# Optimization experiments

Hardware: AMD Instinct MI355X
Metric: run time of the kernel (lower is better)

Reference implementation:

```python
import jax, jax.numpy as jnp
import numpy as np
import math

INPUT_DIM = 256
HIDDEN_DIM = 128  # per-head dim
NUM_HEAD = 8
N = 1024          # seq len == variables
BATCH = 8
C = HIDDEN_DIM * NUM_HEAD  # 1024


def setup_inputs() -> dict:
    key = jax.random.key(0)
    ks = jax.random.split(key, 11)
    s = 0.02
    return {
        "x": jax.random.normal(ks[0], (BATCH, N, INPUT_DIM), dtype=jnp.float32),
        "B_bias": jax.random.normal(ks[1], (N, N), dtype=jnp.float32),
        "wq_w": jax.random.normal(ks[2], (INPUT_DIM, C), dtype=jnp.float32) * s,
        "wq_b": jax.random.normal(ks[3], (C,), dtype=jnp.float32) * s,
        "wk_w": jax.random.normal(ks[4], (INPUT_DIM, C), dtype=jnp.float32) * s,
        "wk_b": jax.random.normal(ks[5], (C,), dtype=jnp.float32) * s,
        "wv_w": jax.random.normal(ks[6], (INPUT_DIM, C), dtype=jnp.float32) * s,
        "wv_b": jax.random.normal(ks[7], (C,), dtype=jnp.float32) * s,
        "proj_w": jax.random.normal(ks[8], (C, HIDDEN_DIM), dtype=jnp.float32) * s,
        "proj_b": jax.random.normal(ks[9], (HIDDEN_DIM,), dtype=jnp.float32) * s,
    }


def reference(x, B_bias, wq_w, wq_b, wk_w, wk_b, wv_w, wv_b, proj_w, proj_b):
    B, n, _ = x.shape
    sdk = jnp.float32(math.sqrt(HIDDEN_DIM))
    # projections -> [B, N, C], split heads -> [B, H, N, h]
    def heads(y):
        return y.reshape(B, n, NUM_HEAD, HIDDEN_DIM).transpose(0, 2, 1, 3)
    q = heads(x @ wq_w + wq_b)
    k = heads(x @ wk_w + wk_b)
    v = heads(x @ wv_w + wv_b)
    # scores [B, H, N, N] with learned additive bias (broadcast over B, H)
    scores = jnp.einsum("bhnd,bhmd->bhnm", q, k) / sdk + B_bias
    attn = jax.nn.softmax(scores, axis=-1)
    out = jnp.einsum("bhnm,bhmd->bhnd", attn, v)  # [B, H, N, h]
    out = out.transpose(0, 2, 1, 3).reshape(B, n, C)
    return out @ proj_w + proj_b
```

## Files before the change

kernel.cpp:

```cpp
#include <hip/hip_runtime.h>
#include <math.h>

#define SEQ  1024
#define IND  256
#define CC   1024
#define NH   8
#define HD   128
#define BH   64

typedef __bf16 bf16x8 __attribute__((ext_vector_type(8)));
typedef __bf16 bf16x4 __attribute__((ext_vector_type(4)));
typedef float  f32x4  __attribute__((ext_vector_type(4)));
typedef unsigned short u16;

static constexpr float RSDK = 0.08838834764831845f;

__device__ __forceinline__ u16 f2bf(float f) {
    unsigned int u = __float_as_uint(f);
    u += 0x7fffu + ((u >> 16) & 1u);
    return (u16)(u >> 16);
}

__global__ __launch_bounds__(256) void prep_kernel(
    const float* __restrict__ x, u16* __restrict__ xb,
    const float* __restrict__ w0, const float* __restrict__ w1, const float* __restrict__ w2,
    u16* __restrict__ o0, u16* __restrict__ o1, u16* __restrict__ o2,
    const float* __restrict__ pw, u16* __restrict__ pT)
{
    __shared__ float tile[32][33];
    const int id = blockIdx.x;

    if (id < 2048) {
        const int i = id * 256 + threadIdx.x;
        float4 v = ((const float4*)x)[i];
        ushort4 o;
        o.x = f2bf(v.x); o.y = f2bf(v.y); o.z = f2bf(v.z); o.w = f2bf(v.w);
        ((ushort4*)xb)[i] = o;
        return;
    }

    const float* in; u16* out; int R, C, c0, r0;
    if (id < 2816) {
        const int rem = id - 2048;
        const int z = rem >> 8;
        const int rem2 = rem & 255;
        in  = (z == 0) ? w0 : (z == 1) ? w1 : w2;
        out = (z == 0) ? o0 : (z == 1) ? o1 : o2;
        R = IND; C = CC;
        c0 = (rem2 & 31) * 32;
        r0 = (rem2 >> 5) * 32;
    } else {
        const int rem = id - 2816;
        in = pw; out = pT;
        R = CC; C = HD;
        c0 = (rem & 3) * 32;
        r0 = (rem >> 2) * 32;
    }

    const int row = threadIdx.x >> 3, col4 = (threadIdx.x & 7) * 4;
    float4 v = *(const float4*)&in[(size_t)(r0 + row) * C + c0 + col4];
    tile[row][col4 + 0] = v.x; tile[row][col4 + 1] = v.y;
    tile[row][col4 + 2] = v.z; tile[row][col4 + 3] = v.w;
    __syncthreads();
    ushort4 o;
    o.x = f2bf(tile[col4 + 0][row]);
    o.y = f2bf(tile[col4 + 1][row]);
    o.z = f2bf(tile[col4 + 2][row]);
    o.w = f2bf(tile[col4 + 3][row]);
    *(ushort4*)&out[(size_t)(c0 + row) * R + r0 + col4] = o;
}

#define QKV_LDW 72
__global__ __launch_bounds__(256) void qkv_kernel(
    const u16* __restrict__ xb,
    const u16* __restrict__ wT0, const u16* __restrict__ wT1, const u16* __restrict__ wT2,
    const float* __restrict__ b0, const float* __restrict__ b1, const float* __restrict__ b2,
    u16* __restrict__ q_out, u16* __restrict__ k_out, u16* __restrict__ vt_out)
{
    const int mat = blockIdx.z;
    const u16* wT  = (mat == 0) ? wT0 : (mat == 1) ? wT1 : wT2;
    const float* wb = (mat == 0) ? b0 : (mat == 1) ? b1 : b2;
    const float scale = (mat == 0) ? RSDK : 1.0f;

    __shared__ __align__(16) u16 As[128 * QKV_LDW];
    __shared__ __align__(16) u16 Bs[128 * QKV_LDW];

    const int tid = threadIdx.x;
    const int lane = tid & 63, wave = tid >> 6;
    const int ln = lane & 15, quad = lane >> 4;
    const int m0 = blockIdx.x * 128;
    const int n0 = blockIdx.y * 128;
    const int wm = (wave & 1) * 64;
    const int wn = (wave >> 1) * 64;

    f32x4 acc[4][4];
    #pragma unroll
    for (int mb = 0; mb < 4; ++mb)
        #pragma unroll
        for (int nb = 0; nb < 4; ++nb)
            #pragma unroll
            for (int r = 0; r < 4; ++r) acc[mb][nb][r] = 0.0f;

    const int r8 = tid >> 3, pb8 = tid & 7;

    const u16* ag = xb + (size_t)(m0 + r8) * IND + pb8 * 8;
    const u16* bg = wT + (size_t)(n0 + r8) * IND + pb8 * 8;

    bf16x8 pa[4], pbv[4];
    #pragma unroll
    for (int c = 0; c < 4; ++c) {
        pa[c]  = *(const bf16x8*)(ag + (size_t)c * 32 * IND);
        pbv[c] = *(const bf16x8*)(bg + (size_t)c * 32 * IND);
    }

    for (int kt = 0; kt < 4; ++kt) {
        __syncthreads();
        #pragma unroll
        for (int c = 0; c < 4; ++c) {
            *(bf16x8*)(As + (size_t)(c * 32 + r8) * QKV_LDW + pb8 * 8) = pa[c];
            *(bf16x8*)(Bs + (size_t)(c * 32 + r8) * QKV_LDW + pb8 * 8) = pbv[c];
        }
        __syncthreads();
        if (kt < 3) {
            #pragma unroll
            for (int c = 0; c < 4; ++c) {
                pa[c]  = *(const bf16x8*)(ag + (size_t)c * 32 * IND + (kt + 1) * 64);
                pbv[c] = *(const bf16x8*)(bg + (size_t)c * 32 * IND + (kt + 1) * 64);
            }
        }
        #pragma unroll
        for (int ks = 0; ks < 2; ++ks) {
            bf16x8 af[4], bf[4];
            #pragma unroll
            for (int mb = 0; mb < 4; ++mb)
                af[mb] = *(const bf16x8*)(As + (size_t)(wm + mb * 16 + ln) * QKV_LDW
                                             + (ks * 4 + quad) * 8);
            #pragma unroll
            for (int nb = 0; nb < 4; ++nb)
                bf[nb] = *(const bf16x8*)(Bs + (size_t)(wn + nb * 16 + ln) * QKV_LDW
                                             + (ks * 4 + quad) * 8);
            #pragma unroll
            for (int mb = 0; mb < 4; ++mb)
                #pragma unroll
                for (int nb = 0; nb < 4; ++nb)
                    acc[mb][nb] = __builtin_amdgcn_mfma_f32_16x16x32_bf16(
                        af[mb], bf[nb], acc[mb][nb], 0, 0, 0);
        }
    }

    if (mat != 2) {
        u16* outp = (mat == 0) ? q_out : k_out;
        #pragma unroll
        for (int nb = 0; nb < 4; ++nb) {
            const int c = n0 + wn + nb * 16 + ln;
            const float bv = wb[c];
            const int h = c >> 7, d = c & 127;
            #pragma unroll
            for (int mb = 0; mb < 4; ++mb) {
                #pragma unroll
                for (int r = 0; r < 4; ++r) {
                    const int m = m0 + wm + mb * 16 + quad * 4 + r;
                    const int b = m >> 10, tok = m & 1023;
                    outp[((size_t)(b * NH + h) * SEQ + tok) * HD + d] =
                        f2bf((acc[mb][nb][r] + bv) * scale);
                }
            }
        }
    } else {
        #pragma unroll
        for (int nb = 0; nb < 4; ++nb) {
            const int c = n0 + wn + nb * 16 + ln;
            const float bv = wb[c];
            const int h = c >> 7, d = c & 127;
            #pragma unroll
            for (int mb = 0; mb < 4; ++mb) {
                const int m = m0 + wm + mb * 16 + quad * 4;
                const int b = m >> 10, tok0 = m & 1023;
                ushort4 o;
                o.x = f2bf(acc[mb][nb][0] + bv);
                o.y = f2bf(acc[mb][nb][1] + bv);
                o.z = f2bf(acc[mb][nb][2] + bv);
                o.w = f2bf(acc[mb][nb][3] + bv);
                *(ushort4*)&vt_out[((size_t)(b * NH + h) * HD + d) * SEQ + tok0] = o;
            }
        }
    }
}

#define KVB    32
#define KS_LDW 136
#define VS_LDW 40
#define PL_LDW 36
__global__ __launch_bounds__(256) void attn_kernel(
    const u16* __restrict__ Q, const u16* __restrict__ K,
    const u16* __restrict__ Vt, const float* __restrict__ bias,
    u16* __restrict__ aout)
{
    __shared__ __align__(16) u16 Ks[KVB * KS_LDW];
    __shared__ __align__(16) u16 Vs[128 * VS_LDW];
    __shared__ __align__(16) u16 Pl[4][16 * PL_LDW];

    const int tid = threadIdx.x;
    const int lane = tid & 63, wave = tid >> 6;
    const int ln = lane & 15, quad = lane >> 4;
    const int bh = blockIdx.x;
    const int q0 = blockIdx.y * 64 + wave * 16;

    bf16x8 qf[4];
    {
        const u16* qp = Q + ((size_t)bh * SEQ + q0 + ln) * HD + quad * 8;
        #pragma unroll
        for (int ks = 0; ks < 4; ++ks) qf[ks] = *(const bf16x8*)(qp + ks * 32);
    }

    f32x4 Oa[8];
    #pragma unroll
    for (int db = 0; db < 8; ++db)
        #pragma unroll
        for (int r = 0; r < 4; ++r) Oa[db][r] = 0.0f;
    float l_i[4] = {0.0f, 0.0f, 0.0f, 0.0f};

    u16* ppw = &Pl[wave][0];
    const u16* Kg0 = K  + (size_t)bh * SEQ * HD;
    const u16* Vg0 = Vt + (size_t)bh * HD * SEQ;
    const float* brow0 = bias + (size_t)(q0 + quad * 4) * SEQ + ln;

    const int r16 = tid >> 4, pb16 = tid & 15;
    const int r4  = tid >> 2, pb4  = tid & 3;

    const u16* kg = Kg0 + (size_t)r16 * HD + pb16 * 8;
    const u16* vg = Vg0 + (size_t)r4 * SEQ + pb4 * 8;

    bf16x8 kp[2], vp[2];
    #pragma unroll
    for (int c = 0; c < 2; ++c) {
        kp[c] = *(const bf16x8*)(kg + (size_t)c * 16 * HD);
        vp[c] = *(const bf16x8*)(vg + (size_t)c * 64 * SEQ);
    }

    float bpre[2][4];
    #pragma unroll
    for (int nb = 0; nb < 2; ++nb)
        #pragma unroll
        for (int r = 0; r < 4; ++r)
            bpre[nb][r] = brow0[(size_t)r * SEQ + nb * 16];

    for (int kt = 0; kt < 32; ++kt) {
        __syncthreads();
        #pragma unroll
        for (int c = 0; c < 2; ++c) {
            *(bf16x8*)(Ks + (size_t)(c * 16 + r16) * KS_LDW + pb16 * 8) = kp[c];
            *(bf16x8*)(Vs + (size_t)(c * 64 + r4) * VS_LDW + pb4 * 8)   = vp[c];
        }
        __syncthreads();

        if (kt < 31) {
            #pragma unroll
            for (int c = 0; c < 2; ++c) {
                kp[c] = *(const bf16x8*)(kg + (size_t)(kt + 1) * KVB * HD + (size_t)c * 16 * HD);
                vp[c] = *(const bf16x8*)(vg + (size_t)c * 64 * SEQ + (kt + 1) * KVB);
            }
        }

        #pragma unroll
        for (int nb = 0; nb < 2; ++nb) {
            const u16* kr = Ks + (size_t)(nb * 16 + ln) * KS_LDW;
            bf16x8 kf[4];
            #pragma unroll
            for (int ks = 0; ks < 4; ++ks)
                kf[ks] = *(const bf16x8*)(kr + (ks * 4 + quad) * 8);
            f32x4 s;
            #pragma unroll
            for (int r = 0; r < 4; ++r) s[r] = 0.0f;
            #pragma unroll
            for (int ks = 0; ks < 4; ++ks)
                s = __builtin_amdgcn_mfma_f32_16x16x32_bf16(qf[ks], kf[ks], s, 0, 0, 0);
            #pragma unroll
            for (int r = 0; r < 4; ++r) {
                const float p = __expf(s[r] + bpre[nb][r]);
                l_i[r] += p;
                ppw[(quad * 4 + r) * PL_LDW + nb * 16 + ln] = f2bf(p);
            }
        }

        if (kt < 31) {
            #pragma unroll
            for (int nb = 0; nb < 2; ++nb)
                #pragma unroll
                for (int r = 0; r < 4; ++r)
                    bpre[nb][r] = brow0[(size_t)r * SEQ + (kt + 1) * KVB + nb * 16];
        }

        bf16x8 af;
        {
            const u16* pr = ppw + ln * PL_LDW + quad * 8;
            bf16x4 lo = *(const bf16x4*)(pr);
            bf16x4 hi = *(const bf16x4*)(pr + 4);
            #pragma unroll
            for (int j = 0; j < 4; ++j) { af[j] = lo[j]; af[4 + j] = hi[j]; }
        }

        #pragma unroll
        for (int db = 0; db < 8; ++db) {
            bf16x8 vf = *(const bf16x8*)(Vs + (size_t)(db * 16 + ln) * VS_LDW + quad * 8);
            Oa[db] = __builtin_amdgcn_mfma_f32_16x16x32_bf16(af, vf, Oa[db], 0, 0, 0);
        }
    }

    const int b = bh >> 3, h = bh & 7;
    #pragma unroll
    for (int r = 0; r < 4; ++r) {
        float v = l_i[r];
        #pragma unroll
        for (int off = 1; off < 16; off <<= 1) v += __shfl_xor(v, off);
        const float inv = 1.0f / v;
        const int tok = q0 + quad * 4 + r;
        u16* op = aout + ((size_t)(b * SEQ + tok)) * CC + h * HD + ln;
        #pragma unroll
        for (int db = 0; db < 8; ++db) op[db * 16] = f2bf(Oa[db][r] * inv);
    }
}

__global__ __launch_bounds__(256) void proj_kernel(
    const u16* __restrict__ A, const u16* __restrict__ pT,
    const float* __restrict__ pb, float* __restrict__ out)
{
    __shared__ float Rs[3][16 * 132];
    const int tid = threadIdx.x;
    const int lane = tid & 63, kh = tid >> 6;
    const int ln = lane & 15, quad = lane >> 4;
    const int m0 = blockIdx.x * 16;

    f32x4 acc[8];
    #pragma unroll
    for (int nb = 0; nb < 8; ++nb)
        #pragma unroll
        for (int r = 0; r < 4; ++r) acc[nb][r] = 0.0f;

    const u16* ap = A  + (size_t)(m0 + ln) * CC + kh * 256 + quad * 8;
    const u16* bp = pT + (size_t)ln * CC + kh * 256 + quad * 8;

    #pragma unroll
    for (int kt = 0; kt < 8; ++kt) {
        bf16x8 af = *(const bf16x8*)(ap + kt * 32);
        #pragma unroll
        for (int nb = 0; nb < 8; ++nb) {
            bf16x8 bf = *(const bf16x8*)(bp + (size_t)nb * 16 * CC + kt * 32);
            acc[nb] = __builtin_amdgcn_mfma_f32_16x16x32_bf16(af, bf, acc[nb], 0, 0, 0);
        }
    }

    if (kh > 0) {
        #pragma unroll
        for (int nb = 0; nb < 8; ++nb)
            #pragma unroll
            for (int r = 0; r < 4; ++r)
                Rs[kh - 1][(quad * 4 + r) * 132 + nb * 16 + ln] = acc[nb][r];
    }
    __syncthreads();
    if (kh == 0) {
        #pragma unroll
        for (int nb = 0; nb < 8; ++nb) {
            const int c = nb * 16 + ln;
            const float bv = pb[c];
            #pragma unroll
            for (int r = 0; r < 4; ++r) {
                const int ri = (quad * 4 + r) * 132 + c;
                out[(size_t)(m0 + quad * 4 + r) * HD + c] =
                    acc[nb][r] + Rs[0][ri] + Rs[1][ri] + Rs[2][ri] + bv;
            }
        }
    }
}

extern "C" void kernel_launch(void* const* d_in, const int* in_sizes, int n_in,
                              void* d_out, int out_size, void* d_ws, size_t ws_size,
                              hipStream_t stream)
{
    const float* x    = (const float*)d_in[0];
    const float* bias = (const float*)d_in[1];
    const float* wq   = (const float*)d_in[2];
    const float* wqb  = (const float*)d_in[3];
    const float* wk   = (const float*)d_in[4];
    const float* wkb  = (const float*)d_in[5];
    const float* wv   = (const float*)d_in[6];
    const float* wvb  = (const float*)d_in[7];
    const float* pw   = (const float*)d_in[8];
    const float* pb   = (const float*)d_in[9];
    float* out = (float*)d_out;

    u16* ws = (u16*)d_ws;
    size_t off = 0;
    u16* xb  = ws + off; off += (size_t)8192 * IND;
    u16* wqT = ws + off; off += (size_t)CC * IND;
    u16* wkT = ws + off; off += (size_t)CC * IND;
    u16* wvT = ws + off; off += (size_t)CC * IND;
    u16* pT  = ws + off; off += (size_t)HD * CC;
    u16* Qw  = ws + off; off += (size_t)BH * SEQ * HD;
    u16* Kw  = ws + off; off += (size_t)BH * SEQ * HD;
    u16* Vtw = ws + off; off += (size_t)BH * HD * SEQ;
    u16* Aw  = ws + off; off += (size_t)8192 * CC;

    prep_kernel<<<2944, 256, 0, stream>>>(x, xb, wq, wk, wv, wqT, wkT, wvT, pw, pT);
    qkv_kernel<<<dim3(64, 8, 3), 256, 0, stream>>>(
        xb, wqT, wkT, wvT, wqb, wkb, wvb, Qw, Kw, Vtw);
    attn_kernel<<<dim3(64, 16), 256, 0, stream>>>(Qw, Kw, Vtw, bias, Aw);
    proj_kernel<<<512, 256, 0, stream>>>(Aw, pT, pb, out);
}
```

Baseline: 190.3 us.

## Transpose QK^T MFMA and build P operand in registers via permlane swaps

```diff
diff --git a/kernel.cpp b/kernel.cpp
--- a/kernel.cpp
+++ b/kernel.cpp
@@ -19,6 +19,12 @@
     unsigned int u = __float_as_uint(f);
     u += 0x7fffu + ((u >> 16) & 1u);
     return (u16)(u >> 16);
+}
+
+__device__ __forceinline__ unsigned cvt_pk_bf16(float lo, float hi) {
+    unsigned r;
+    asm("v_cvt_pk_bf16_f32 %0, %1, %2" : "=v"(r) : "v"(lo), "v"(hi));
+    return r;
 }
 
 __global__ __launch_bounds__(256) void prep_kernel(
@@ -190,15 +196,13 @@
 #define KVB    32
 #define KS_LDW 136
 #define VS_LDW 40
-#define PL_LDW 36
-__global__ __launch_bounds__(256) void attn_kernel(
+__global__ __launch_bounds__(256, 4) void attn_kernel(
     const u16* __restrict__ Q, const u16* __restrict__ K,
     const u16* __restrict__ Vt, const float* __restrict__ bias,
     u16* __restrict__ aout)
 {
     __shared__ __align__(16) u16 Ks[KVB * KS_LDW];
     __shared__ __align__(16) u16 Vs[128 * VS_LDW];
-    __shared__ __align__(16) u16 Pl[4][16 * PL_LDW];
 
     const int tid = threadIdx.x;
     const int lane = tid & 63, wave = tid >> 6;
@@ -218,12 +222,11 @@
     for (int db = 0; db < 8; ++db)
         #pragma unroll
         for (int r = 0; r < 4; ++r) Oa[db][r] = 0.0f;
-    float l_i[4] = {0.0f, 0.0f, 0.0f, 0.0f};
-
-    u16* ppw = &Pl[wave][0];
+    float l_loc = 0.0f;
+
     const u16* Kg0 = K  + (size_t)bh * SEQ * HD;
     const u16* Vg0 = Vt + (size_t)bh * HD * SEQ;
-    const float* brow0 = bias + (size_t)(q0 + quad * 4) * SEQ + ln;
+    const float* brow = bias + (size_t)(q0 + ln) * SEQ + quad * 4;
 
     const int r16 = tid >> 4, pb16 = tid & 15;
     const int r4  = tid >> 2, pb4  = tid & 3;
@@ -238,12 +241,10 @@
         vp[c] = *(const bf16x8*)(vg + (size_t)c * 64 * SEQ);
     }
 
-    float bpre[2][4];
+    float4 bpre[2];
     #pragma unroll
     for (int nb = 0; nb < 2; ++nb)
-        #pragma unroll
-        for (int r = 0; r < 4; ++r)
-            bpre[nb][r] = brow0[(size_t)r * SEQ + nb * 16];
+        bpre[nb] = *(const float4*)(brow + nb * 16);
 
     for (int kt = 0; kt < 32; ++kt) {
         __syncthreads();
@@ -262,6 +263,7 @@
             }
         }
 
+        float p8[2][4];
         #pragma unroll
         for (int nb = 0; nb < 2; ++nb) {
             const u16* kr = Ks + (size_t)(nb * 16 + ln) * KS_LDW;
@@ -274,31 +276,32 @@
             for (int r = 0; r < 4; ++r) s[r] = 0.0f;
             #pragma unroll
             for (int ks = 0; ks < 4; ++ks)
-                s = __builtin_amdgcn_mfma_f32_16x16x32_bf16(qf[ks], kf[ks], s, 0, 0, 0);
+                s = __builtin_amdgcn_mfma_f32_16x16x32_bf16(kf[ks], qf[ks], s, 0, 0, 0);
             #pragma unroll
             for (int r = 0; r < 4; ++r) {
                 const float p = __expf(s[r] + bpre[nb][r]);
-                l_i[r] += p;
-                ppw[(quad * 4 + r) * PL_LDW + nb * 16 + ln] = f2bf(p);
+                l_loc += p;
+                p8[nb][r] = p;
             }
         }
 
         if (kt < 31) {
             #pragma unroll
             for (int nb = 0; nb < 2; ++nb)
-                #pragma unroll
-                for (int r = 0; r < 4; ++r)
-                    bpre[nb][r] = brow0[(size_t)r * SEQ + (kt + 1) * KVB + nb * 16];
-        }
-
-        bf16x8 af;
-        {
-            const u16* pr = ppw + ln * PL_LDW + quad * 8;
-            bf16x4 lo = *(const bf16x4*)(pr);
-            bf16x4 hi = *(const bf16x4*)(pr + 4);
-            #pragma unroll
-            for (int j = 0; j < 4; ++j) { af[j] = lo[j]; af[4 + j] = hi[j]; }
-        }
+                bpre[nb] = *(const float4*)(brow + (kt + 1) * KVB + nb * 16);
+        }
+
+        unsigned x0 = cvt_pk_bf16(p8[0][0], p8[0][1]);
+        unsigned x1 = cvt_pk_bf16(p8[0][2], p8[0][3]);
+        unsigned y0 = cvt_pk_bf16(p8[1][0], p8[1][1]);
+        unsigned y1 = cvt_pk_bf16(p8[1][2], p8[1][3]);
+        asm("v_permlane32_swap_b32 %0, %1" : "+v"(x0), "+v"(y0));
+        asm("v_permlane32_swap_b32 %0, %1" : "+v"(x1), "+v"(y1));
+        asm("v_permlane16_swap_b32 %0, %1" : "+v"(x0), "+v"(y0));
+        asm("v_permlane16_swap_b32 %0, %1" : "+v"(x1), "+v"(y1));
+        union { unsigned u[4]; bf16x8 v; } afu;
+        afu.u[0] = x0; afu.u[1] = x1; afu.u[2] = y0; afu.u[3] = y1;
+        const bf16x8 af = afu.v;
 
         #pragma unroll
         for (int db = 0; db < 8; ++db) {
@@ -307,13 +310,14 @@
         }
     }
 
+    float ltot = l_loc;
+    ltot += __shfl_xor(ltot, 16);
+    ltot += __shfl_xor(ltot, 32);
+
     const int b = bh >> 3, h = bh & 7;
     #pragma unroll
     for (int r = 0; r < 4; ++r) {
-        float v = l_i[r];
-        #pragma unroll
-        for (int off = 1; off < 16; off <<= 1) v += __shfl_xor(v, off);
-        const float inv = 1.0f / v;
+        const float inv = 1.0f / __shfl(ltot, quad * 4 + r);
         const int tok = q0 + quad * 4 + r;
         u16* op = aout + ((size_t)(b * SEQ + tok)) * CC + h * HD + ln;
         #pragma unroll
```

Measured after the change: 181.8 us. -4.5%, faster.
